# Performance work log

Hardware: AMD Instinct MI355X
Metric: run time of the kernel (lower is better)

## Reference

```python
import jax, jax.numpy as jnp
import numpy as np

B, S, E, H = 2, 2048, 1024, 16
D = E // H  # head_dim = 64


def setup_inputs() -> dict:
    key = jax.random.key(0)
    ks = jax.random.split(key, 14)
    inp = {
        "query": jax.random.normal(ks[0], (B, S, E), jnp.float32),
        "key": jax.random.normal(ks[1], (B, S, E), jnp.float32),
        "value": jax.random.normal(ks[2], (B, S, E), jnp.float32),
        "adj": jax.random.normal(ks[3], (S, S), jnp.float32),
        "mask": jax.random.randint(ks[4], (B, 1, S, S), 0, 2, jnp.int32),
    }
    sc = 1.0 / np.sqrt(E)
    inp["Wq"] = jax.random.normal(ks[5], (E, E), jnp.float32) * sc
    inp["bq"] = jax.random.normal(ks[6], (E,), jnp.float32) * sc
    inp["Wk"] = jax.random.normal(ks[7], (E, E), jnp.float32) * sc
    inp["bk"] = jax.random.normal(ks[8], (E,), jnp.float32) * sc
    inp["Wv"] = jax.random.normal(ks[9], (E, E), jnp.float32) * sc
    inp["bv"] = jax.random.normal(ks[10], (E,), jnp.float32) * sc
    inp["Wo"] = jax.random.normal(ks[11], (E, E), jnp.float32) * sc
    inp["bo"] = jax.random.normal(ks[12], (E,), jnp.float32) * sc
    return inp


def reference(query, key, value, adj, mask, Wq, bq, Wk, bk, Wv, bv, Wo, bo):
    b, s, _ = query.shape
    # projections, split into heads: [B,S,E] -> [B,H,S,D]
    def heads(x, W, bias):
        y = jnp.einsum("bse,ef->bsf", x, W.T) + bias
        return y.reshape(b, s, H, D).transpose(0, 2, 1, 3)

    Q = heads(query, Wq, bq)
    K = heads(key, Wk, bk)
    V = heads(value, Wv, bv)

    # scores: [B,H,S,S], scaled by sqrt(head_dim), plus adjacency bias
    scores = jnp.einsum("bhqd,bhkd->bhqk", Q, K) / jnp.sqrt(jnp.float32(D))
    scores = scores + adj[None, None, :, :]
    scores = jnp.where(mask == 0, jnp.float32(-jnp.inf), scores)

    weights = jax.nn.softmax(scores, axis=-1)
    out = jnp.einsum("bhqk,bhkd->bhqd", weights, V)
    out = out.transpose(0, 2, 1, 3).reshape(b, s, E)
    return jnp.einsum("bse,ef->bsf", out, Wo.T) + bo
```

## Files before the change

### kernel.cpp

```cpp
#include <hip/hip_runtime.h>


typedef unsigned short ushort_t;
typedef __attribute__((ext_vector_type(8))) short bf16x8;
typedef __attribute__((ext_vector_type(4))) float floatx4;

#define NB 2
#define NS 2048
#define NE 1024
#define NH 16
#define ND 64

__device__ __forceinline__ unsigned short f2bf(float f) {
  unsigned int u = __float_as_uint(f);
  return (unsigned short)((u + 0x7fffu + ((u >> 16) & 1u)) >> 16);
}
__device__ __forceinline__ float bf2f(unsigned short h) {
  return __uint_as_float(((unsigned int)h) << 16);
}

__device__ __forceinline__ void gload_lds16(const void* g, void* l) {
  __builtin_amdgcn_global_load_lds(
      (const __attribute__((address_space(1))) unsigned int*)g,
      (__attribute__((address_space(3))) unsigned int*)l, 16, 0, 0);
}

__global__ __launch_bounds__(256) void convert_kernel(
    const float* __restrict__ q, const float* __restrict__ k, const float* __restrict__ v,
    const float* __restrict__ wq, const float* __restrict__ wk,
    const float* __restrict__ wv, const float* __restrict__ wo,
    const float* __restrict__ adj, const int* __restrict__ mask,
    ushort_t* __restrict__ qb, ushort_t* __restrict__ kb, ushort_t* __restrict__ vb,
    ushort_t* __restrict__ wqb, ushort_t* __restrict__ wkb,
    ushort_t* __restrict__ wvb, ushort_t* __restrict__ wob,
    ushort_t* __restrict__ bias)
{
  const long U1 = (long)NB * NS * NE / 8;
  const long U2 = (long)NE * NE / 8;
  long idx = (long)blockIdx.x * 256 + threadIdx.x;
  const float* src;
  ushort_t* dst;
  if (idx < U1) { src = q; dst = qb; }
  else if ((idx -= U1) < U1) { src = k; dst = kb; }
  else if ((idx -= U1) < U1) { src = v; dst = vb; }
  else if ((idx -= U1) < U2) { src = wq; dst = wqb; }
  else if ((idx -= U2) < U2) { src = wk; dst = wkb; }
  else if ((idx -= U2) < U2) { src = wv; dst = wvb; }
  else if ((idx -= U2) < U2) { src = wo; dst = wob; }
  else {
    idx -= U2;
    long flat = idx * 8;
    long rem = flat & ((1L << 22) - 1);
    const float4* a4 = (const float4*)(adj + rem);
    const int4* m4 = (const int4*)(mask + flat);
    float4 a0 = a4[0], a1 = a4[1];
    int4 m0 = m4[0], m1 = m4[1];
    const float NEGV = -1e30f;
    union { ushort_t us[8]; uint4 v4; } o;
    o.us[0] = f2bf(m0.x ? a0.x : NEGV);
    o.us[1] = f2bf(m0.y ? a0.y : NEGV);
    o.us[2] = f2bf(m0.z ? a0.z : NEGV);
    o.us[3] = f2bf(m0.w ? a0.w : NEGV);
    o.us[4] = f2bf(m1.x ? a1.x : NEGV);
    o.us[5] = f2bf(m1.y ? a1.y : NEGV);
    o.us[6] = f2bf(m1.z ? a1.z : NEGV);
    o.us[7] = f2bf(m1.w ? a1.w : NEGV);
    ((uint4*)bias)[idx] = o.v4;
    return;
  }
  const float4* s4 = (const float4*)src;
  float4 a0 = s4[idx * 2], a1 = s4[idx * 2 + 1];
  union { ushort_t us[8]; uint4 v4; } o;
  o.us[0] = f2bf(a0.x); o.us[1] = f2bf(a0.y); o.us[2] = f2bf(a0.z); o.us[3] = f2bf(a0.w);
  o.us[4] = f2bf(a1.x); o.us[5] = f2bf(a1.y); o.us[6] = f2bf(a1.z); o.us[7] = f2bf(a1.w);
  ((uint4*)dst)[idx] = o.v4;
}

__global__ __launch_bounds__(256) void qkv_kernel(
    const ushort_t* __restrict__ xq, const ushort_t* __restrict__ xk, const ushort_t* __restrict__ xv,
    const ushort_t* __restrict__ wqb, const ushort_t* __restrict__ wkb, const ushort_t* __restrict__ wvb,
    const float* __restrict__ bq, const float* __restrict__ bk, const float* __restrict__ bvv,
    ushort_t* __restrict__ Qh, ushort_t* __restrict__ Kh, ushort_t* __restrict__ Vt)
{
  __shared__ __align__(16) ushort_t As[128 * 32];
  __shared__ __align__(16) ushort_t Bs[128 * 32];

  int z = blockIdx.z;
  const ushort_t* X = (z == 0) ? xq : (z == 1) ? xk : xv;
  const ushort_t* W = (z == 0) ? wqb : (z == 1) ? wkb : wvb;
  const float* bias = (z == 0) ? bq : (z == 1) ? bk : bvv;

  int t = threadIdx.x;
  int lane = t & 63, w = t >> 6;
  int quad = lane >> 4, l16 = lane & 15;
  int wr = w >> 1, wc = w & 1;
  int m0 = blockIdx.y * 128, f0 = blockIdx.x * 128;

  floatx4 acc[4][4] = {};

  int arow = t >> 2, apart = t & 3;
  const ushort_t* Xg = X + (long)(m0 + arow) * NE + apart * 8;
  const ushort_t* Wg = W + (long)(f0 + arow) * NE + apart * 8;
  ushort_t* As_t = As + t * 8;
  ushort_t* Bs_t = Bs + t * 8;

  for (int k0 = 0; k0 < NE; k0 += 32) {
    __syncthreads();
    gload_lds16(Xg + k0, As_t);
    gload_lds16(Xg + k0 + 64 * NE, As_t + 64 * 32);
    gload_lds16(Wg + k0, Bs_t);
    gload_lds16(Wg + k0 + 64 * NE, Bs_t + 64 * 32);
    __syncthreads();
    bf16x8 af[4], bf[4];
#pragma unroll
    for (int i = 0; i < 4; i++)
      af[i] = *(const bf16x8*)(As + (wr * 64 + i * 16 + l16) * 32 + quad * 8);
#pragma unroll
    for (int j = 0; j < 4; j++)
      bf[j] = *(const bf16x8*)(Bs + (wc * 64 + j * 16 + l16) * 32 + quad * 8);
#pragma unroll
    for (int i = 0; i < 4; i++)
#pragma unroll
      for (int j = 0; j < 4; j++)
        acc[i][j] = __builtin_amdgcn_mfma_f32_16x16x32_bf16(af[i], bf[j], acc[i][j], 0, 0, 0);
  }

  ushort_t* Out = (z == 0) ? Qh : (z == 1) ? Kh : Vt;
  bool isV = (z == 2);
#pragma unroll
  for (int j = 0; j < 4; j++) {
    int f = f0 + wc * 64 + j * 16 + l16;
    float bval = bias[f];
    int h = f >> 6, d = f & 63;
#pragma unroll
    for (int i = 0; i < 4; i++) {
      int mbase = m0 + wr * 64 + i * 16 + quad * 4;
#pragma unroll
      for (int r = 0; r < 4; r++) {
        int m = mbase + r;
        int b = m >> 11, s = m & 2047;
        float y = acc[i][j][r] + bval;
        long off;
        if (!isV) off = ((long)(b * NH + h) * NS + s) * ND + d;
        else      off = ((long)(b * NH + h) * ND + d) * NS + s;
        Out[off] = f2bf(y);
      }
    }
  }
}

__global__ __launch_bounds__(256) void attn_kernel(
    const ushort_t* __restrict__ Qh, const ushort_t* __restrict__ Kh,
    const ushort_t* __restrict__ Vt, const ushort_t* __restrict__ bias,
    ushort_t* __restrict__ aout)
{
  __shared__ __align__(16) ushort_t Qs[64 * 64];
  __shared__ __align__(16) ushort_t Ks[32 * 64];
  __shared__ __align__(16) ushort_t Vts[64 * 32];
  __shared__ __align__(16) ushort_t Ps[4][16 * 72];

  int t = threadIdx.x, lane = t & 63, w = t >> 6;
  int quad = lane >> 4, l16 = lane & 15;
  int qt = blockIdx.x;
  int bh = blockIdx.y;
  int bb = bh >> 4, h = bh & 15;
  int q0 = qt * 64;

  const ushort_t* Qg = Qh + ((long)bh * NS + q0) * ND;
#pragma unroll
  for (int c = 0; c < 2; c++) {
    int idx = c * 256 + t;
    int row = idx >> 3, part = idx & 7;
    gload_lds16(Qg + (long)row * ND + part * 8, Qs + idx * 8);
  }
  __syncthreads();

  bf16x8 aq[2];
#pragma unroll
  for (int kd = 0; kd < 2; kd++)
    aq[kd] = *(const bf16x8*)(Qs + (w * 16 + l16) * 64 + kd * 32 + quad * 8);

  floatx4 acc[4] = {};
  float lsum[4] = {0.f, 0.f, 0.f, 0.f};

  const ushort_t* Kg = Kh + (long)bh * NS * ND;
  const ushort_t* Vg = Vt + (long)bh * ND * NS;
  const ushort_t* biasg = bias + (long)bb * NS * NS;

  int krow = t >> 3, kpart = t & 7;
  int vrow = t >> 2, vpart = t & 3;

  for (int kt = 0; kt < NS / 32; kt++) {
    int k0 = kt * 32;
    __syncthreads();
    gload_lds16(Kg + (long)(k0 + krow) * ND + kpart * 8, Ks + t * 8);
    gload_lds16(Vg + (long)vrow * NS + k0 + vpart * 8, Vts + t * 8);
    __syncthreads();

    bf16x8 bk[2][2];
#pragma unroll
    for (int jk = 0; jk < 2; jk++)
#pragma unroll
      for (int kd = 0; kd < 2; kd++)
        bk[jk][kd] = *(const bf16x8*)(Ks + (jk * 16 + l16) * 64 + kd * 32 + quad * 8);
    floatx4 sc[2] = {};
#pragma unroll
    for (int jk = 0; jk < 2; jk++)
#pragma unroll
      for (int kd = 0; kd < 2; kd++)
        sc[jk] = __builtin_amdgcn_mfma_f32_16x16x32_bf16(aq[kd], bk[jk][kd], sc[jk], 0, 0, 0);

    int qg = q0 + w * 16 + quad * 4;
    float bsv[2][4];
#pragma unroll
    for (int r = 0; r < 4; r++)
#pragma unroll
      for (int jk = 0; jk < 2; jk++)
        bsv[jk][r] = bf2f(biasg[(long)(qg + r) * NS + k0 + jk * 16 + l16]);
    float p[2][4];
#pragma unroll
    for (int r = 0; r < 4; r++) {
      float s0 = sc[0][r] * 0.125f + bsv[0][r];
      float s1 = sc[1][r] * 0.125f + bsv[1][r];
      float p0 = __expf(s0);
      float p1 = __expf(s1);
      lsum[r] += p0 + p1;
      p[0][r] = p0;
      p[1][r] = p1;
    }

#pragma unroll
    for (int jk = 0; jk < 2; jk++)
#pragma unroll
      for (int r = 0; r < 4; r++)
        Ps[w][(quad * 4 + r) * 72 + jk * 16 + l16] = f2bf(p[jk][r]);
    asm volatile("s_waitcnt lgkmcnt(0)" ::: "memory");

    bf16x8 ap = *(const bf16x8*)(&Ps[w][l16 * 72 + quad * 8]);
    bf16x8 bv[4];
#pragma unroll
    for (int j = 0; j < 4; j++)
      bv[j] = *(const bf16x8*)(Vts + (j * 16 + l16) * 32 + quad * 8);
#pragma unroll
    for (int j = 0; j < 4; j++)
      acc[j] = __builtin_amdgcn_mfma_f32_16x16x32_bf16(ap, bv[j], acc[j], 0, 0, 0);
  }

#pragma unroll
  for (int r = 0; r < 4; r++) {
    float s = lsum[r];
    s += __shfl_xor(s, 1);
    s += __shfl_xor(s, 2);
    s += __shfl_xor(s, 4);
    s += __shfl_xor(s, 8);
    lsum[r] = s;
  }

  ushort_t* og = aout + (long)bb * NS * NE + h * ND;
#pragma unroll
  for (int r = 0; r < 4; r++) {
    int qg = q0 + w * 16 + quad * 4 + r;
    float inv = 1.0f / lsum[r];
#pragma unroll
    for (int j = 0; j < 4; j++) {
      int d = j * 16 + l16;
      og[(long)qg * NE + d] = f2bf(acc[j][r] * inv);
    }
  }
}

__global__ __launch_bounds__(256) void oproj_kernel(
    const ushort_t* __restrict__ A, const ushort_t* __restrict__ Wob,
    const float* __restrict__ bo, float* __restrict__ out)
{
  __shared__ __align__(16) ushort_t As[128 * 32];
  __shared__ __align__(16) ushort_t Bs[64 * 32];

  int t = threadIdx.x;
  int lane = t & 63, w = t >> 6;
  int quad = lane >> 4, l16 = lane & 15;
  int wr = w >> 1, wc = w & 1;
  int m0 = blockIdx.y * 128, f0 = blockIdx.x * 64;

  floatx4 acc[4][2] = {};
  int arow = t >> 2, apart = t & 3;
  const ushort_t* Xg = A + (long)(m0 + arow) * NE + apart * 8;
  const ushort_t* Wg = Wob + (long)(f0 + arow) * NE + apart * 8;
  ushort_t* As_t = As + t * 8;
  ushort_t* Bs_t = Bs + t * 8;
  bool bstage = (arow < 64);

  for (int k0 = 0; k0 < NE; k0 += 32) {
    __syncthreads();
    gload_lds16(Xg + k0, As_t);
    gload_lds16(Xg + k0 + 64 * NE, As_t + 64 * 32);
    if (bstage) gload_lds16(Wg + k0, Bs_t);
    __syncthreads();
    bf16x8 af[4], bf[2];
#pragma unroll
    for (int i = 0; i < 4; i++)
      af[i] = *(const bf16x8*)(As + (wr * 64 + i * 16 + l16) * 32 + quad * 8);
#pragma unroll
    for (int j = 0; j < 2; j++)
      bf[j] = *(const bf16x8*)(Bs + (wc * 32 + j * 16 + l16) * 32 + quad * 8);
#pragma unroll
    for (int i = 0; i < 4; i++)
#pragma unroll
      for (int j = 0; j < 2; j++)
        acc[i][j] = __builtin_amdgcn_mfma_f32_16x16x32_bf16(af[i], bf[j], acc[i][j], 0, 0, 0);
  }

#pragma unroll
  for (int j = 0; j < 2; j++) {
    int f = f0 + wc * 32 + j * 16 + l16;
    float bval = bo[f];
#pragma unroll
    for (int i = 0; i < 4; i++) {
      int mbase = m0 + wr * 64 + i * 16 + quad * 4;
#pragma unroll
      for (int r = 0; r < 4; r++) {
        int m = mbase + r;
        out[(long)m * NE + f] = acc[i][j][r] + bval;
      }
    }
  }
}

extern "C" void kernel_launch(void* const* d_in, const int* in_sizes, int n_in,
                              void* d_out, int out_size, void* d_ws, size_t ws_size,
                              hipStream_t stream) {
  const float* query = (const float*)d_in[0];
  const float* key   = (const float*)d_in[1];
  const float* value = (const float*)d_in[2];
  const float* adj   = (const float*)d_in[3];
  const int*   mask  = (const int*)d_in[4];
  const float* Wq = (const float*)d_in[5];
  const float* bq = (const float*)d_in[6];
  const float* Wk = (const float*)d_in[7];
  const float* bk = (const float*)d_in[8];
  const float* Wv = (const float*)d_in[9];
  const float* bv = (const float*)d_in[10];
  const float* Wo = (const float*)d_in[11];
  const float* bo = (const float*)d_in[12];
  float* out = (float*)d_out;

  char* ws = (char*)d_ws;
  const size_t MB = 1ull << 20;
  ushort_t* qb   = (ushort_t*)(ws + 0 * MB);
  ushort_t* kb   = (ushort_t*)(ws + 8 * MB);
  ushort_t* vb   = (ushort_t*)(ws + 16 * MB);
  ushort_t* wqb  = (ushort_t*)(ws + 24 * MB);
  ushort_t* wkb  = (ushort_t*)(ws + 26 * MB);
  ushort_t* wvb  = (ushort_t*)(ws + 28 * MB);
  ushort_t* wob  = (ushort_t*)(ws + 30 * MB);
  ushort_t* Qh   = (ushort_t*)(ws + 32 * MB);
  ushort_t* Kh   = (ushort_t*)(ws + 40 * MB);
  ushort_t* Vt   = (ushort_t*)(ws + 48 * MB);
  ushort_t* aout = (ushort_t*)(ws + 56 * MB);
  ushort_t* bias = (ushort_t*)(ws + 64 * MB);

  convert_kernel<<<12288, 256, 0, stream>>>(query, key, value, Wq, Wk, Wv, Wo,
                                            adj, mask, qb, kb, vb, wqb, wkb, wvb, wob, bias);
  qkv_kernel<<<dim3(8, 32, 3), 256, 0, stream>>>(qb, kb, vb, wqb, wkb, wvb,
                                                 bq, bk, bv, Qh, Kh, Vt);
  attn_kernel<<<dim3(32, 32), 256, 0, stream>>>(Qh, Kh, Vt, bias, aout);
  oproj_kernel<<<dim3(16, 32), 256, 0, stream>>>(aout, wob, bo, out);
}
```

Before: 315.2 us.

## Transpose attention bias and load K/V fragments directly from global memory

```diff
diff --git a/kernel.cpp b/kernel.cpp
--- a/kernel.cpp
+++ b/kernel.cpp
@@ -29,11 +29,9 @@
     const float* __restrict__ q, const float* __restrict__ k, const float* __restrict__ v,
     const float* __restrict__ wq, const float* __restrict__ wk,
     const float* __restrict__ wv, const float* __restrict__ wo,
-    const float* __restrict__ adj, const int* __restrict__ mask,
     ushort_t* __restrict__ qb, ushort_t* __restrict__ kb, ushort_t* __restrict__ vb,
     ushort_t* __restrict__ wqb, ushort_t* __restrict__ wkb,
-    ushort_t* __restrict__ wvb, ushort_t* __restrict__ wob,
-    ushort_t* __restrict__ bias)
+    ushort_t* __restrict__ wvb, ushort_t* __restrict__ wob)
 {
   const long U1 = (long)NB * NS * NE / 8;
   const long U2 = (long)NE * NE / 8;
@@ -46,34 +44,50 @@
   else if ((idx -= U1) < U2) { src = wq; dst = wqb; }
   else if ((idx -= U2) < U2) { src = wk; dst = wkb; }
   else if ((idx -= U2) < U2) { src = wv; dst = wvb; }
-  else if ((idx -= U2) < U2) { src = wo; dst = wob; }
-  else {
-    idx -= U2;
-    long flat = idx * 8;
-    long rem = flat & ((1L << 22) - 1);
-    const float4* a4 = (const float4*)(adj + rem);
-    const int4* m4 = (const int4*)(mask + flat);
-    float4 a0 = a4[0], a1 = a4[1];
-    int4 m0 = m4[0], m1 = m4[1];
-    const float NEGV = -1e30f;
-    union { ushort_t us[8]; uint4 v4; } o;
-    o.us[0] = f2bf(m0.x ? a0.x : NEGV);
-    o.us[1] = f2bf(m0.y ? a0.y : NEGV);
-    o.us[2] = f2bf(m0.z ? a0.z : NEGV);
-    o.us[3] = f2bf(m0.w ? a0.w : NEGV);
-    o.us[4] = f2bf(m1.x ? a1.x : NEGV);
-    o.us[5] = f2bf(m1.y ? a1.y : NEGV);
-    o.us[6] = f2bf(m1.z ? a1.z : NEGV);
-    o.us[7] = f2bf(m1.w ? a1.w : NEGV);
-    ((uint4*)bias)[idx] = o.v4;
-    return;
-  }
+  else { idx -= U2; src = wo; dst = wob; }
   const float4* s4 = (const float4*)src;
   float4 a0 = s4[idx * 2], a1 = s4[idx * 2 + 1];
   union { ushort_t us[8]; uint4 v4; } o;
   o.us[0] = f2bf(a0.x); o.us[1] = f2bf(a0.y); o.us[2] = f2bf(a0.z); o.us[3] = f2bf(a0.w);
   o.us[4] = f2bf(a1.x); o.us[5] = f2bf(a1.y); o.us[6] = f2bf(a1.z); o.us[7] = f2bf(a1.w);
   ((uint4*)dst)[idx] = o.v4;
+}
+
+__global__ __launch_bounds__(256) void bias_kernel(
+    const float* __restrict__ adj, const int* __restrict__ mask,
+    ushort_t* __restrict__ bias_t)
+{
+  __shared__ ushort_t Ts[64][68];
+  int t = threadIdx.x;
+  int k0 = blockIdx.x * 64, q0 = blockIdx.y * 64, b = blockIdx.z;
+  const long mbase = (long)b * NS * NS;
+  int qr = t >> 4;
+  int kc = (t & 15) * 4;
+#pragma unroll
+  for (int rr = 0; rr < 4; rr++) {
+    int qq = qr + rr * 16;
+    float4 a = *(const float4*)(adj + (long)(q0 + qq) * NS + k0 + kc);
+    int4 m = *(const int4*)(mask + mbase + (long)(q0 + qq) * NS + k0 + kc);
+    ushort4 o;
+    o.x = f2bf(m.x ? a.x : -1e30f);
+    o.y = f2bf(m.y ? a.y : -1e30f);
+    o.z = f2bf(m.z ? a.z : -1e30f);
+    o.w = f2bf(m.w ? a.w : -1e30f);
+    *(ushort4*)(&Ts[qq][kc]) = o;
+  }
+  __syncthreads();
+  int kr = t >> 4;
+  int qc = (t & 15) * 4;
+#pragma unroll
+  for (int rr = 0; rr < 4; rr++) {
+    int kk = kr + rr * 16;
+    ushort4 o;
+    o.x = Ts[qc + 0][kk];
+    o.y = Ts[qc + 1][kk];
+    o.z = Ts[qc + 2][kk];
+    o.w = Ts[qc + 3][kk];
+    *(ushort4*)(bias_t + mbase + (long)(k0 + kk) * NS + q0 + qc) = o;
+  }
 }
 
 __global__ __launch_bounds__(256) void qkv_kernel(
@@ -149,14 +163,12 @@
   }
 }
 
-__global__ __launch_bounds__(256) void attn_kernel(
+__global__ __launch_bounds__(256, 4) void attn_kernel(
     const ushort_t* __restrict__ Qh, const ushort_t* __restrict__ Kh,
-    const ushort_t* __restrict__ Vt, const ushort_t* __restrict__ bias,
+    const ushort_t* __restrict__ Vt, const ushort_t* __restrict__ bias_t,
     ushort_t* __restrict__ aout)
 {
   __shared__ __align__(16) ushort_t Qs[64 * 64];
-  __shared__ __align__(16) ushort_t Ks[32 * 64];
-  __shared__ __align__(16) ushort_t Vts[64 * 32];
   __shared__ __align__(16) ushort_t Ps[4][16 * 72];
 
   int t = threadIdx.x, lane = t & 63, w = t >> 6;
@@ -183,26 +195,31 @@
   floatx4 acc[4] = {};
   float lsum[4] = {0.f, 0.f, 0.f, 0.f};
 
-  const ushort_t* Kg = Kh + (long)bh * NS * ND;
-  const ushort_t* Vg = Vt + (long)bh * ND * NS;
-  const ushort_t* biasg = bias + (long)bb * NS * NS;
-
-  int krow = t >> 3, kpart = t & 7;
-  int vrow = t >> 2, vpart = t & 3;
+  const ushort_t* Kf = Kh + (long)bh * NS * ND + (long)l16 * ND + quad * 8;
+  const ushort_t* Vf = Vt + (long)bh * ND * NS + (long)l16 * NS + quad * 8;
+  const ushort_t* Bf = bias_t + (long)bb * NS * NS + (long)l16 * NS
+                       + q0 + w * 16 + quad * 4;
+  ushort_t* Psw = &Ps[w][0];
 
   for (int kt = 0; kt < NS / 32; kt++) {
     int k0 = kt * 32;
-    __syncthreads();
-    gload_lds16(Kg + (long)(k0 + krow) * ND + kpart * 8, Ks + t * 8);
-    gload_lds16(Vg + (long)vrow * NS + k0 + vpart * 8, Vts + t * 8);
-    __syncthreads();
 
     bf16x8 bk[2][2];
 #pragma unroll
     for (int jk = 0; jk < 2; jk++)
 #pragma unroll
       for (int kd = 0; kd < 2; kd++)
-        bk[jk][kd] = *(const bf16x8*)(Ks + (jk * 16 + l16) * 64 + kd * 32 + quad * 8);
+        bk[jk][kd] = *(const bf16x8*)(Kf + (long)(k0 + jk * 16) * ND + kd * 32);
+
+    bf16x8 bv[4];
+#pragma unroll
+    for (int j = 0; j < 4; j++)
+      bv[j] = *(const bf16x8*)(Vf + (long)(j * 16) * NS + k0);
+
+    ushort_t bsa[2][4];
+    *(ushort4*)bsa[0] = *(const ushort4*)(Bf + (long)k0 * NS);
+    *(ushort4*)bsa[1] = *(const ushort4*)(Bf + (long)(k0 + 16) * NS);
+
     floatx4 sc[2] = {};
 #pragma unroll
     for (int jk = 0; jk < 2; jk++)
@@ -210,18 +227,11 @@
       for (int kd = 0; kd < 2; kd++)
         sc[jk] = __builtin_amdgcn_mfma_f32_16x16x32_bf16(aq[kd], bk[jk][kd], sc[jk], 0, 0, 0);
 
-    int qg = q0 + w * 16 + quad * 4;
-    float bsv[2][4];
-#pragma unroll
-    for (int r = 0; r < 4; r++)
-#pragma unroll
-      for (int jk = 0; jk < 2; jk++)
-        bsv[jk][r] = bf2f(biasg[(long)(qg + r) * NS + k0 + jk * 16 + l16]);
     float p[2][4];
 #pragma unroll
     for (int r = 0; r < 4; r++) {
-      float s0 = sc[0][r] * 0.125f + bsv[0][r];
-      float s1 = sc[1][r] * 0.125f + bsv[1][r];
+      float s0 = sc[0][r] * 0.125f + bf2f(bsa[0][r]);
+      float s1 = sc[1][r] * 0.125f + bf2f(bsa[1][r]);
       float p0 = __expf(s0);
       float p1 = __expf(s1);
       lsum[r] += p0 + p1;
@@ -233,14 +243,10 @@
     for (int jk = 0; jk < 2; jk++)
 #pragma unroll
       for (int r = 0; r < 4; r++)
-        Ps[w][(quad * 4 + r) * 72 + jk * 16 + l16] = f2bf(p[jk][r]);
+        Psw[(quad * 4 + r) * 72 + jk * 16 + l16] = f2bf(p[jk][r]);
     asm volatile("s_waitcnt lgkmcnt(0)" ::: "memory");
 
-    bf16x8 ap = *(const bf16x8*)(&Ps[w][l16 * 72 + quad * 8]);
-    bf16x8 bv[4];
-#pragma unroll
-    for (int j = 0; j < 4; j++)
-      bv[j] = *(const bf16x8*)(Vts + (j * 16 + l16) * 32 + quad * 8);
+    bf16x8 ap = *(const bf16x8*)(Psw + l16 * 72 + quad * 8);
 #pragma unroll
     for (int j = 0; j < 4; j++)
       acc[j] = __builtin_amdgcn_mfma_f32_16x16x32_bf16(ap, bv[j], acc[j], 0, 0, 0);
@@ -359,8 +365,9 @@
   ushort_t* aout = (ushort_t*)(ws + 56 * MB);
   ushort_t* bias = (ushort_t*)(ws + 64 * MB);
 
-  convert_kernel<<<12288, 256, 0, stream>>>(query, key, value, Wq, Wk, Wv, Wo,
-                                            adj, mask, qb, kb, vb, wqb, wkb, wvb, wob, bias);
+  convert_kernel<<<8192, 256, 0, stream>>>(query, key, value, Wq, Wk, Wv, Wo,
+                                           qb, kb, vb, wqb, wkb, wvb, wob);
+  bias_kernel<<<dim3(32, 32, 2), 256, 0, stream>>>(adj, mask, bias);
   qkv_kernel<<<dim3(8, 32, 3), 256, 0, stream>>>(qb, kb, vb, wqb, wkb, wvb,
                                                  bq, bk, bv, Qh, Kh, Vt);
   attn_kernel<<<dim3(32, 32), 256, 0, stream>>>(Qh, Kh, Vt, bias, aout);
```

After: 510.5 us. +62.0%, slower.
